# Kernel tuning notes

Measured on AMD Instinct MI355X. Metric: run time of the kernel, lower is better.

## Reference

```python
import jax, jax.numpy as jnp
import numpy as np


def setup_inputs() -> dict:
    key = jax.random.key(0)
    k1, k2, k3 = jax.random.split(key, 3)
    N, E, D = 50000, 800000, 64
    h = jax.random.normal(k1, (N, D), dtype=jnp.float32)
    src = jax.random.randint(k2, (E,), 0, N, dtype=jnp.int64)
    dst = jax.random.randint(k3, (E,), 0, N, dtype=jnp.int64)
    return {"h": h, "src": src, "dst": dst}


def reference(h, src, dst):
    # u_dot_v: per-edge dot product of source and destination node embeddings,
    # then sigmoid. Equivalent to DGL apply_edges(fn.u_dot_v('h','h','score')).
    score = jnp.sum(h[src] * h[dst], axis=-1)  # [E]
    return jax.nn.sigmoid(score)
```

## Files before the change

### kernel.cpp

```cpp
#include <hip/hip_runtime.h>
#include <hip/hip_fp16.h>
#include <math.h>


#define DOT_D 64

typedef int   v4i __attribute__((ext_vector_type(4)));
typedef float v4f __attribute__((ext_vector_type(4)));

__global__ __launch_bounds__(256) void f32_to_f16_kernel(
    const float* __restrict__ h, __half2* __restrict__ hh, int n4)
{
    int i = blockIdx.x * blockDim.x + threadIdx.x;
    if (i >= n4) return;
    float4 v = ((const float4*)h)[i];
    hh[2 * i]     = __floats2half2_rn(v.x, v.y);
    hh[2 * i + 1] = __floats2half2_rn(v.z, v.w);
}

__global__ __launch_bounds__(256) void dot_sigmoid_f16_mlp_kernel(
    const __half* __restrict__ h,
    const int* __restrict__ src,
    const int* __restrict__ dst,
    float* __restrict__ out,
    int E)
{
    int tid  = blockIdx.x * blockDim.x + threadIdx.x;
    int lane = tid & 7;
    int g    = tid >> 3;
    int eb   = g << 2;
    if (eb >= E) return;

    if (eb + 3 < E) {
        v4i s4 = __builtin_nontemporal_load((const v4i*)(src + eb));
        v4i d4 = __builtin_nontemporal_load((const v4i*)(dst + eb));
        int ss[4] = { s4.x, s4.y, s4.z, s4.w };
        int dd[4] = { d4.x, d4.y, d4.z, d4.w };

        float4 ur[4], vr[4];
#pragma unroll
        for (int i = 0; i < 4; ++i) {
            ur[i] = ((const float4*)(h + (size_t)ss[i] * DOT_D))[lane];
            vr[i] = ((const float4*)(h + (size_t)dd[i] * DOT_D))[lane];
        }

        v4f res;
#pragma unroll
        for (int i = 0; i < 4; ++i) {
            const __half2* up = (const __half2*)&ur[i];
            const __half2* vp = (const __half2*)&vr[i];
            float p = 0.0f;
#pragma unroll
            for (int k = 0; k < 4; ++k) {
                float2 uf = __half22float2(up[k]);
                float2 vf = __half22float2(vp[k]);
                p = fmaf(uf.x, vf.x, p);
                p = fmaf(uf.y, vf.y, p);
            }
            p += __shfl_xor(p, 4);
            p += __shfl_xor(p, 2);
            p += __shfl_xor(p, 1);
            res[i] = 1.0f / (1.0f + __expf(-p));
        }

        if (lane == 0) {
            __builtin_nontemporal_store(res, (v4f*)(out + eb));
        }
    } else {
        for (int i = 0; i < 4; ++i) {
            int e = eb + i;
            if (e >= E) break;
            int s = src[e];
            int d = dst[e];
            float4 ur = ((const float4*)(h + (size_t)s * DOT_D))[lane];
            float4 vr = ((const float4*)(h + (size_t)d * DOT_D))[lane];
            const __half2* up = (const __half2*)&ur;
            const __half2* vp = (const __half2*)&vr;
            float p = 0.0f;
#pragma unroll
            for (int k = 0; k < 4; ++k) {
                float2 uf = __half22float2(up[k]);
                float2 vf = __half22float2(vp[k]);
                p = fmaf(uf.x, vf.x, p);
                p = fmaf(uf.y, vf.y, p);
            }
            p += __shfl_xor(p, 4);
            p += __shfl_xor(p, 2);
            p += __shfl_xor(p, 1);
            if (lane == 0) out[e] = 1.0f / (1.0f + __expf(-p));
        }
    }
}

__global__ __launch_bounds__(256) void dot_sigmoid_f32_kernel(
    const float* __restrict__ h,
    const int* __restrict__ src,
    const int* __restrict__ dst,
    float* __restrict__ out,
    int E)
{
    int tid  = blockIdx.x * blockDim.x + threadIdx.x;
    int lane = tid & 15;
    int e    = tid >> 4;
    if (e >= E) return;

    int s = src[e];
    int d = dst[e];
    float4 u = ((const float4*)(h + (size_t)s * DOT_D))[lane];
    float4 v = ((const float4*)(h + (size_t)d * DOT_D))[lane];
    float p = u.x * v.x + u.y * v.y + u.z * v.z + u.w * v.w;
    p += __shfl_xor(p, 8);
    p += __shfl_xor(p, 4);
    p += __shfl_xor(p, 2);
    p += __shfl_xor(p, 1);
    if (lane == 0) out[e] = 1.0f / (1.0f + __expf(-p));
}

extern "C" void kernel_launch(void* const* d_in, const int* in_sizes, int n_in,
                              void* d_out, int out_size, void* d_ws, size_t ws_size,
                              hipStream_t stream) {
    const float* h   = (const float*)d_in[0];
    const int*   src = (const int*)d_in[1];
    const int*   dst = (const int*)d_in[2];
    float*       out = (float*)d_out;

    int ND = in_sizes[0];
    int E  = in_sizes[1];
    size_t f16_bytes = (size_t)ND * sizeof(__half);

    if (ws_size >= f16_bytes) {
        __half* hh = (__half*)d_ws;
        int n4 = ND / 4;
        f32_to_f16_kernel<<<(n4 + 255) / 256, 256, 0, stream>>>(h, (__half2*)hh, n4);

        long long groups = (E + 3) / 4;
        long long total_threads = groups * 8;
        int grid = (int)((total_threads + 255) / 256);
        dot_sigmoid_f16_mlp_kernel<<<grid, 256, 0, stream>>>(hh, src, dst, out, E);
    } else {
        long long total_threads = (long long)E * 16;
        int grid = (int)((total_threads + 255) / 256);
        dot_sigmoid_f32_kernel<<<grid, 256, 0, stream>>>(h, src, dst, out, E);
    }
}
```

Measured before the change: 84.83 us.

## Fuse fp16 conversion and edge dot into one cooperative persistent kernel

Merges the fp32-to-fp16 conversion kernel and the gather-dot-sigmoid kernel into a single cooperative launch of 1024 blocks. A grid-wide sync separates the conversion pass from the edge pass, and both passes use grid-stride loops. The aim is to remove one kernel launch and the gap between kernels. In exchange it adds the cost of a grid barrier and the overhead of a cooperative launch, and it caps parallelism at a fixed persistent grid, which may reduce memory-level parallelism for the random gathers.

New measurement: 170.3 us. +100.8%, slower.

```diff
diff --git a/kernel.cpp b/kernel.cpp
--- a/kernel.cpp
+++ b/kernel.cpp
@@ -1,6 +1,9 @@
 #include <hip/hip_runtime.h>
 #include <hip/hip_fp16.h>
+#include <hip/hip_cooperative_groups.h>
 #include <math.h>
+
+namespace cg = cooperative_groups;
 
 
 #define DOT_D 64
@@ -8,86 +11,97 @@
 typedef int   v4i __attribute__((ext_vector_type(4)));
 typedef float v4f __attribute__((ext_vector_type(4)));
 
-__global__ __launch_bounds__(256) void f32_to_f16_kernel(
-    const float* __restrict__ h, __half2* __restrict__ hh, int n4)
-{
-    int i = blockIdx.x * blockDim.x + threadIdx.x;
-    if (i >= n4) return;
-    float4 v = ((const float4*)h)[i];
-    hh[2 * i]     = __floats2half2_rn(v.x, v.y);
-    hh[2 * i + 1] = __floats2half2_rn(v.z, v.w);
-}
-
-__global__ __launch_bounds__(256) void dot_sigmoid_f16_mlp_kernel(
-    const __half* __restrict__ h,
+__global__ __launch_bounds__(256, 4) void fused_conv_dot_kernel(
+    const float* __restrict__ h,
     const int* __restrict__ src,
     const int* __restrict__ dst,
     float* __restrict__ out,
+    __half* __restrict__ hh,
+    int n8,
     int E)
 {
-    int tid  = blockIdx.x * blockDim.x + threadIdx.x;
-    int lane = tid & 7;
-    int g    = tid >> 3;
-    int eb   = g << 2;
-    if (eb >= E) return;
+    const int nthreads = gridDim.x * blockDim.x;
+    const int tid = blockIdx.x * blockDim.x + threadIdx.x;
 
-    if (eb + 3 < E) {
-        v4i s4 = __builtin_nontemporal_load((const v4i*)(src + eb));
-        v4i d4 = __builtin_nontemporal_load((const v4i*)(dst + eb));
-        int ss[4] = { s4.x, s4.y, s4.z, s4.w };
-        int dd[4] = { d4.x, d4.y, d4.z, d4.w };
+    for (int i = tid; i < n8; i += nthreads) {
+        float4 a = ((const float4*)h)[2 * i];
+        float4 b = ((const float4*)h)[2 * i + 1];
+        __half2 o[4];
+        o[0] = __floats2half2_rn(a.x, a.y);
+        o[1] = __floats2half2_rn(a.z, a.w);
+        o[2] = __floats2half2_rn(b.x, b.y);
+        o[3] = __floats2half2_rn(b.z, b.w);
+        ((v4f*)hh)[i] = *(v4f*)o;
+    }
 
-        float4 ur[4], vr[4];
+    cg::this_grid().sync();
+
+    const int lane = tid & 7;
+    const int g0   = tid >> 3;
+    const int gstride = nthreads >> 3;
+    const int ngroups = (E + 3) >> 2;
+
+    for (int g = g0; g < ngroups; g += gstride) {
+        int eb = g << 2;
+
+        if (eb + 3 < E) {
+            v4i s4 = __builtin_nontemporal_load((const v4i*)(src + eb));
+            v4i d4 = __builtin_nontemporal_load((const v4i*)(dst + eb));
+            int ss[4] = { s4.x, s4.y, s4.z, s4.w };
+            int dd[4] = { d4.x, d4.y, d4.z, d4.w };
+
+            float4 ur[4], vr[4];
 #pragma unroll
-        for (int i = 0; i < 4; ++i) {
-            ur[i] = ((const float4*)(h + (size_t)ss[i] * DOT_D))[lane];
-            vr[i] = ((const float4*)(h + (size_t)dd[i] * DOT_D))[lane];
-        }
+            for (int i = 0; i < 4; ++i) {
+                ur[i] = ((const float4*)(hh + (size_t)ss[i] * DOT_D))[lane];
+                vr[i] = ((const float4*)(hh + (size_t)dd[i] * DOT_D))[lane];
+            }
 
-        v4f res;
+            v4f res;
 #pragma unroll
-        for (int i = 0; i < 4; ++i) {
-            const __half2* up = (const __half2*)&ur[i];
-            const __half2* vp = (const __half2*)&vr[i];
-            float p = 0.0f;
+            for (int i = 0; i < 4; ++i) {
+                const __half2* up = (const __half2*)&ur[i];
+                const __half2* vp = (const __half2*)&vr[i];
+                float p = 0.0f;
 #pragma unroll
-            for (int k = 0; k < 4; ++k) {
-                float2 uf = __half22float2(up[k]);
-                float2 vf = __half22float2(vp[k]);
-                p = fmaf(uf.x, vf.x, p);
-                p = fmaf(uf.y, vf.y, p);
+                for (int k = 0; k < 4; ++k) {
+                    float2 uf = __half22float2(up[k]);
+                    float2 vf = __half22float2(vp[k]);
+                    p = fmaf(uf.x, vf.x, p);
+                    p = fmaf(uf.y, vf.y, p);
+                }
+                p += __shfl_xor(p, 4);
+                p += __shfl_xor(p, 2);
+                p += __shfl_xor(p, 1);
+                res[i] = 1.0f / (1.0f + __expf(-p));
             }
-            p += __shfl_xor(p, 4);
-            p += __shfl_xor(p, 2);
-            p += __shfl_xor(p, 1);
-            res[i] = 1.0f / (1.0f + __expf(-p));
-        }
 
-        if (lane == 0) {
-            __builtin_nontemporal_store(res, (v4f*)(out + eb));
-        }
-    } else {
-        for (int i = 0; i < 4; ++i) {
-            int e = eb + i;
-            if (e >= E) break;
-            int s = src[e];
-            int d = dst[e];
-            float4 ur = ((const float4*)(h + (size_t)s * DOT_D))[lane];
-            float4 vr = ((const float4*)(h + (size_t)d * DOT_D))[lane];
-            const __half2* up = (const __half2*)&ur;
-            const __half2* vp = (const __half2*)&vr;
-            float p = 0.0f;
+            if (lane == 0) {
+                __builtin_nontemporal_store(res, (v4f*)(out + eb));
+            }
+        } else {
+            for (int i = 0; i < 4; ++i) {
+                int e = eb + i;
+                if (e >= E) break;
+                int s = src[e];
+                int d = dst[e];
+                float4 ur = ((const float4*)(hh + (size_t)s * DOT_D))[lane];
+                float4 vr = ((const float4*)(hh + (size_t)d * DOT_D))[lane];
+                const __half2* up = (const __half2*)&ur;
+                const __half2* vp = (const __half2*)&vr;
+                float p = 0.0f;
 #pragma unroll
-            for (int k = 0; k < 4; ++k) {
-                float2 uf = __half22float2(up[k]);
-                float2 vf = __half22float2(vp[k]);
-                p = fmaf(uf.x, vf.x, p);
-                p = fmaf(uf.y, vf.y, p);
+                for (int k = 0; k < 4; ++k) {
+                    float2 uf = __half22float2(up[k]);
+                    float2 vf = __half22float2(vp[k]);
+                    p = fmaf(uf.x, vf.x, p);
+                    p = fmaf(uf.y, vf.y, p);
+                }
+                p += __shfl_xor(p, 4);
+                p += __shfl_xor(p, 2);
+                p += __shfl_xor(p, 1);
+                if (lane == 0) out[e] = 1.0f / (1.0f + __expf(-p));
             }
-            p += __shfl_xor(p, 4);
-            p += __shfl_xor(p, 2);
-            p += __shfl_xor(p, 1);
-            if (lane == 0) out[e] = 1.0f / (1.0f + __expf(-p));
         }
     }
 }
@@ -130,13 +144,12 @@
 
     if (ws_size >= f16_bytes) {
         __half* hh = (__half*)d_ws;
-        int n4 = ND / 4;
-        f32_to_f16_kernel<<<(n4 + 255) / 256, 256, 0, stream>>>(h, (__half2*)hh, n4);
+        int n8 = ND / 8;
 
-        long long groups = (E + 3) / 4;
-        long long total_threads = groups * 8;
-        int grid = (int)((total_threads + 255) / 256);
-        dot_sigmoid_f16_mlp_kernel<<<grid, 256, 0, stream>>>(hh, src, dst, out, E);
+        void* args[] = { (void*)&h, (void*)&src, (void*)&dst, (void*)&out,
+                         (void*)&hh, (void*)&n8, (void*)&E };
+        hipLaunchCooperativeKernel((void*)fused_conv_dot_kernel,
+                                   dim3(1024), dim3(256), args, 0, stream);
     } else {
         long long total_threads = (long long)E * 16;
         int grid = (int)((total_threads + 255) / 256);
```
